# Kernel tuning notes

Hardware: AMD Instinct MI355X
Metric: run time of the kernel (lower is better)

The kernel has to match this reference:

```python
import jax, jax.numpy as jnp
from jax import lax
import numpy as np

# Dims matching init_kwargs / input_specs
B, R, C, CIN, COUT, W, CT = 8, 96, 64, 8, 64, 8, 4


def setup_inputs() -> dict:
    key = jax.random.key(0)
    ks = jax.random.split(key, 16)
    s = 0.05
    n = lambda k, shp: s * jax.random.normal(k, shp, jnp.float32)
    return {
        "x": jax.random.normal(ks[0], (B, R, C, CIN, 1), jnp.float32),
        "x_mark": jax.random.normal(ks[1], (B, R, C, CIN, CT), jnp.float32),
        # hidden_MLP_data: Conv1d(c_in -> c_in*c_out, k=W, groups=c_in) -> per-group in=1
        "Wd": n(ks[2], (CIN * COUT, 1, W)),
        "bd": n(ks[3], (CIN * COUT,)),
        # hidden_MLP_mark: Conv1d(c_in*CT -> c_in*c_out, k=W, groups=c_in) -> per-group in=CT
        "Wm": n(ks[4], (CIN * COUT, CT, W)),
        "bm": n(ks[5], (CIN * COUT,)),
        # gate_data: k=1 grouped conv, per-group 1 -> 2*c_out; stored einsum-friendly [g, 2*c_out]
        "Gd": n(ks[6], (CIN, 2 * COUT)),
        "bgd": n(ks[7], (CIN, 2 * COUT)),
        # gate_mark: per-group CT -> 2*c_out
        "Gm": n(ks[8], (CIN, 2 * COUT, CT)),
        "bgm": n(ks[9], (CIN, 2 * COUT)),
        # gate_hid: per-group c_out -> 2*c_out
        "Gh": n(ks[10], (CIN, 2 * COUT, COUT)),
        "bgh": n(ks[11], (CIN, 2 * COUT)),
        # fc: Conv1d(c_in*c_out -> c_in*c_out, k=seq_R, groups=c_in) -> [g, o, i, R]
        "Fw": n(ks[12], (CIN, COUT, COUT, R)),
        "bf": n(ks[13], (CIN, COUT)),
    }


def _grouped_conv1d(xa, w, b, groups):
    # xa: [N, Cin, L], w: [Cout, Cin//groups, K]
    y = lax.conv_general_dilated(
        xa, w, window_strides=(1,), padding="VALID",
        dimension_numbers=("NCH", "OIH", "NCH"), feature_group_count=groups)
    return y + b[None, :, None]


def reference(x, x_mark, Wd, bd, Wm, bm, Gd, bgd, Gm, bgm, Gh, bgh, Fw, bf):
    Bv, Rv, Cv, cin, _ = x.shape
    ct = x_mark.shape[-1]
    cout = Gh.shape[-1]
    Wk = Wd.shape[-1]

    # ---- deal(): causal windowed grouped conv over R ----
    # pad W zeros in front along R, drop last step -> length R+W-1, VALID conv k=W -> R
    xz = jnp.concatenate([jnp.zeros((Bv, Wk, Cv, cin, 1), x.dtype), x], axis=1)
    xa = xz.transpose(0, 2, 3, 4, 1).reshape(Bv * Cv, cin, Rv + Wk)[:, :, :-1]
    Hd = _grouped_conv1d(xa, Wd, bd, cin)  # [B*C, cin*cout, R]

    mz = jnp.concatenate([jnp.zeros((Bv, Wk, Cv, cin, ct), x.dtype), x_mark], axis=1)
    ma = mz.transpose(0, 2, 3, 4, 1).reshape(Bv * Cv, cin * ct, Rv + Wk)[:, :, :-1]
    Hm = _grouped_conv1d(ma, Wm, bm, cin)

    hid = (Hd + Hm).reshape(Bv, Cv, cin, cout, Rv).transpose(0, 4, 1, 2, 3)  # [B,R,C,cin,cout]

    # ---- gated_unit(): kernel-1 grouped convs == per-group matmuls ----
    xs = x[..., 0]  # [B,R,C,cin]
    g = jnp.einsum("brcg,go->brcgo", xs, Gd) + bgd
    g = g + jnp.einsum("brcgt,got->brcgo", x_mark, Gm) + bgm
    g = g + jnp.einsum("brcgi,goi->brcgo", hid, Gh) + bgh
    sg = jax.nn.sigmoid(g[..., :cout])
    tg = jnp.tanh(g[..., cout:])
    hid = hid * sg + (1.0 - sg) * tg  # [B,R,C,cin,cout]

    # ---- fc: grouped conv with kernel==R -> full contraction over (in-chan, R) ----
    out = jnp.einsum("brcgi,goir->bcgo", hid, Fw) + bf  # [B,C,cin,cout]
    return out
```

## Files before the change

kernel.cpp:

```cpp
#include <hip/hip_runtime.h>
#include <hip/hip_bf16.h>
#include <math.h>

namespace {

typedef __attribute__((ext_vector_type(8))) short bh8;
typedef __attribute__((ext_vector_type(4))) short sh4;
typedef __attribute__((ext_vector_type(4))) float fx4;

constexpr int Rn = 96, Cn = 64, CINn = 8, COUTn = 64;
constexpr int NPOS = 8 * 96 * 64 * 8;
constexpr int PPG  = 8 * 96 * 64;
constexpr float NLOG2E = -1.4426950408889634f;
constexpr float LOG2E2 =  2.8853900817779268f;
constexpr size_t FEAT_OFF = 0;
constexpr size_t FWT_OFF  = (size_t)NPOS * 16;
constexpr size_t CA_OFF   = FWT_OFF + (size_t)NPOS * 16;
constexpr size_t GWT_OFF  = CA_OFF + 65536;
constexpr size_t PART_OFF = GWT_OFF + 196608;

__device__ inline ushort f2b(float f) {
  __hip_bfloat16 h = __float2bfloat16(f);
  return __builtin_bit_cast(ushort, h);
}
__device__ inline int swz8(int bc, int rr, int ib) {
  return (bc * 1024 + rr * 128 + ib) ^ (((rr + bc) & 7) << 4);
}

#define MFMA16(a, b, c) __builtin_amdgcn_mfma_f32_16x16x32_bf16((a), (b), (c), 0, 0, 0)

__global__ __launch_bounds__(512)
void prep_k(const float* __restrict__ x, const float* __restrict__ xm,
            const float* __restrict__ Fw,
            const float* __restrict__ Gd, const float* __restrict__ bgd,
            const float* __restrict__ Gm, const float* __restrict__ bgm,
            const float* __restrict__ bgh,
            const float* __restrict__ Wd, const float* __restrict__ bd,
            const float* __restrict__ Wm, const float* __restrict__ bm,
            ushort* __restrict__ feat, ushort* __restrict__ FwT,
            ushort* __restrict__ GWT, ushort* __restrict__ cA)
{
  __shared__ float tile[64 * 97];
  const int bid = blockIdx.x, t = threadIdx.x;
  if (bid < 768) {
    const int pos = bid * 512 + t;
    const float xs = x[pos];
    const fx4 m = *(const fx4*)(xm + (size_t)pos * 4);
    bh8 o;
    o[0] = (short)f2b(xs);
    o[1] = (short)f2b(m[0]); o[2] = (short)f2b(m[1]);
    o[3] = (short)f2b(m[2]); o[4] = (short)f2b(m[3]);
    o[5] = (short)0x3F80; o[6] = 0; o[7] = 0;
    const int g = pos & 7, pb = pos >> 3;
    *(bh8*)(feat + ((size_t)g * PPG + pb) * 8) = o;
  } else if (bid < 1280) {
    const int go = bid - 768;
    const float* src = Fw + (size_t)go * 6144;
    ushort* dst = FwT + (size_t)go * 6144;
#pragma unroll
    for (int it = 0; it < 12; ++it) {
      const int idx = t + it * 512;
      tile[(idx / 96) * 97 + (idx % 96)] = src[idx];
    }
    __syncthreads();
#pragma unroll
    for (int it = 0; it < 12; ++it) {
      const int idx = t + it * 512;
      const int r = idx >> 6, i = idx & 63;
      dst[idx] = f2b(tile[i * 97 + r]);
    }
  } else if (bid < 1344) {
    const int e = (bid - 1280) * 512 + t;
    const int j = e & 7, lp = (e >> 3) & 63, sub = (e >> 9) & 7, g = e >> 12;
    const int il = lp >> 4, mr = lp & 15;
    const int o2 = (sub >> 2) * 64 + (sub & 3) * 16 + mr;
    float v = 0.f;
    if (il == 0) {
      if (j == 0)      v = Gd[g * 128 + o2];
      else if (j <= 4) v = Gm[(size_t)(g * 128 + o2) * 4 + (j - 1)];
      else if (j == 5) v = bgd[g * 128 + o2] + bgm[g * 128 + o2] + bgh[g * 128 + o2];
    }
    v *= (sub >= 4) ? LOG2E2 : NLOG2E;
    GWT[((size_t)(g * 24 + sub * 3 + 2) * 64 + lp) * 8 + j] = f2b(v);
  } else {
    const int e = (bid - 1344) * 512 + t;
    const int g = e >> 12, co = (e >> 6) & 63, k = e & 63;
    const int tap = k >> 3, tch = k & 7;
    float v = 0.f;
    if (tch == 0)      v = Wd[(g * 64 + co) * 8 + tap];
    else if (tch <= 4) v = Wm[((g * 64 + co) * 4 + (tch - 1)) * 8 + tap];
    else if (tch == 5 && tap == 0) v = bd[g * 64 + co] + bm[g * 64 + co];
    cA[e] = f2b(v);
  }
}

__global__ __launch_bounds__(256)
void gwk(const float* __restrict__ Gh, const float* __restrict__ Wd,
         const float* __restrict__ Wm, const float* __restrict__ bd,
         const float* __restrict__ bm, ushort* __restrict__ GWT)
{
  const int row = blockIdx.x * 4 + (threadIdx.x >> 6);
  const int k = threadIdx.x & 63;
  const int g = row >> 7, o2 = row & 127;
  const int tap = k >> 3, tch = k & 7;
  const float* pA; int sA = 0; float mA = 0.f, mB = 0.f;
  const float* pB;
  if (tch == 0)      { pA = Wd + (size_t)(g * 64) * 8 + tap; sA = 8;  mA = 1.f; }
  else if (tch <= 4) { pA = Wm + ((size_t)(g * 64) * 4 + (tch - 1)) * 8 + tap; sA = 32; mA = 1.f; }
  else if (tch == 5 && tap == 0) { pA = bd + g * 64; sA = 1; mA = 1.f; mB = 1.f; }
  else               { pA = Wd; }
  pB = (mB != 0.f) ? (bm + g * 64) : pA;
  const float* gh = Gh + (size_t)(g * 128 + o2) * 64;
  float acc = 0.f;
#pragma unroll 8
  for (int i = 0; i < 64; ++i) {
    const float wv = fmaf(mB, pB[i], mA * pA[i * sA]);
    acc = fmaf(gh[i], wv, acc);
  }
  acc *= (o2 >= 64) ? LOG2E2 : NLOG2E;
  const int half = o2 >> 6, s = (o2 >> 4) & 3, mr = o2 & 15;
  const int sub = half * 4 + s, fs = k >> 5, lp = ((k & 31) >> 3) * 16 + mr, j = k & 7;
  GWT[((size_t)(g * 24 + sub * 3 + fs) * 64 + lp) * 8 + j] = f2b(acc);
}

__global__ __launch_bounds__(512, 2)
void fused_v10(const ushort* __restrict__ feat, const ushort* __restrict__ FwT,
               const ushort* __restrict__ cA, const ushort* __restrict__ GWT,
               float* __restrict__ part)
{
  __shared__ __align__(16) ushort sTab[16384];
  __shared__ __align__(16) char sGat[2][16384];
  __shared__ float sRed[1024];

  const int t    = threadIdx.x;
  const int lane = t & 63;
  const int w    = t >> 6;
  const int il   = lane >> 4;
  const int mr   = lane & 15;
  const int bid  = blockIdx.x;
  const int g    = bid & 7;
  const int bcT  = (bid >> 3) & 31;
  const int chh  = bid >> 8;
  const ushort* fg = feat + (size_t)g * PPG * 8;
  const int s4   = w & 3, hf = w >> 2;
  const int tb   = lane * 8;

  const int pglob = w * 16 + mr;
  const int cbcl = pglob >> 3, crr = pglob & 7;
  const int cbcg = bcT * 16 + cbcl;
  const int cbb = cbcg >> 6, ccc = cbcg & 63;
  const size_t prow = (size_t)(cbb * 96) * 64 + ccc;

  *(bh8*)&sTab[w * 512 + tb] =
      *(const bh8*)(cA + g * 4096 + ((w >> 1) * 16 + mr) * 64 + (w & 1) * 32 + il * 8);
  {
    const ushort* gsrc = GWT + (size_t)g * 12288;
#pragma unroll
    for (int it = 0; it < 3; ++it) {
      const int idx = it * 512 + t;
      *(bh8*)&sTab[4096 + idx * 8] = *(const bh8*)(gsrc + idx * 8);
    }
  }

  int wadr[4];
#pragma unroll
  for (int s = 0; s < 4; ++s) wadr[s] = swz8(cbcl, crr, s * 32 + il * 8);
  const ushort* fb0 = FwT + ((size_t)(g * 64 + s4 * 16 + mr) * 96) * 64 + 32 * hf + 8 * il;

  fx4 facc = {0.f, 0.f, 0.f, 0.f};
  const bh8 zpad = {0, 0, 0, 0, 0, (short)0x3F80, 0, 0};

  bh8 b0, b1, bx;
  {
    const int r0 = chh * 48;
    const int q0 = r0 + crr - 8 + il;
    const int q1 = q0 + 4;
    b0 = *(const bh8*)(fg + (prow + (size_t)(q0 > 0 ? q0 : 0) * 64) * 8);
    b1 = *(const bh8*)(fg + (prow + (size_t)(q1 > 0 ? q1 : 0) * 64) * 8);
    bx = *(const bh8*)(fg + (prow + (size_t)(r0 + crr) * 64) * 8);
  }
  __syncthreads();

#pragma unroll 1
  for (int k6 = 0; k6 < 6; ++k6) {
    const int r0 = chh * 48 + k6 * 8;
    if (k6 == 0 && chh == 0) {
      if (crr - 8 + il < 0) b0 = zpad;
      if (crr - 4 + il < 0) b1 = zpad;
    }

    fx4 ah[4];
#pragma unroll
    for (int s = 0; s < 4; ++s) {
      const bh8 a0 = *(const bh8*)&sTab[(s * 2 + 0) * 512 + tb];
      const bh8 a1 = *(const bh8*)&sTab[(s * 2 + 1) * 512 + tb];
      fx4 a = {0.f, 0.f, 0.f, 0.f};
      a = MFMA16(a0, b0, a);
      a = MFMA16(a1, b1, a);
      ah[s] = a;
    }

    bh8 b0n = b0, b1n = b1, bxn = bx;
    if (k6 < 5) {
      const int qn = r0 + crr + il;
      b0n = *(const bh8*)(fg + (prow + (size_t)qn * 64) * 8);
      b1n = *(const bh8*)(fg + (prow + (size_t)(qn + 4) * 64) * 8);
      bxn = *(const bh8*)(fg + (prow + (size_t)(r0 + 8 + crr) * 64) * 8);
    }

    char* gbuf = sGat[k6 & 1];
#pragma unroll
    for (int s = 0; s < 4; ++s) {
      const int bs = (8 + s * 3) * 512 + tb;
      const int bt = (8 + (4 + s) * 3) * 512 + tb;
      fx4 aS = {0.f,0.f,0.f,0.f}, aT = {0.f,0.f,0.f,0.f};
      aS = MFMA16(*(const bh8*)&sTab[bs],        b0, aS);
      aS = MFMA16(*(const bh8*)&sTab[bs + 512],  b1, aS);
      aS = MFMA16(*(const bh8*)&sTab[bs + 1024], bx, aS);
      aT = MFMA16(*(const bh8*)&sTab[bt],        b0, aT);
      aT = MFMA16(*(const bh8*)&sTab[bt + 512],  b1, aT);
      aT = MFMA16(*(const bh8*)&sTab[bt + 1024], bx, aT);
      sh4 o4;
#pragma unroll
      for (int cc = 0; cc < 4; ++cc) {
        const float sig = __builtin_amdgcn_rcpf(1.f + exp2f(aS[cc]));
        const float y   = exp2f(aT[cc]);
        const float th  = (y - 1.f) * __builtin_amdgcn_rcpf(y + 1.f);
        o4[cc] = (short)f2b(fmaf(sig, ah[s][cc] - th, th));
      }
      *(sh4*)(gbuf + wadr[s]) = o4;
    }
    __syncthreads();

    {
      const ushort* fb = fb0 + (size_t)r0 * 64;
#pragma unroll
      for (int f = 0; f < 8; ++f) {
        const bh8 aF = *(const bh8*)(fb + f * 64);
        const bh8 bF = *(const bh8*)(gbuf + swz8(mr, f, 64 * hf + 16 * il));
        facc = MFMA16(aF, bF, facc);
      }
    }
    b0 = b0n; b1 = b1n; bx = bxn;
  }

  if (hf == 1) {
#pragma unroll
    for (int cc = 0; cc < 4; ++cc)
      sRed[s4 * 256 + (4 * il + cc) * 16 + mr] = facc[cc];
  }
  __syncthreads();
  if (hf == 0) {
    float* pp = part + ((size_t)(chh * 8 + g) * 32 + bcT) * 1024;
#pragma unroll
    for (int cc = 0; cc < 4; ++cc)
      pp[mr * 64 + s4 * 16 + 4 * il + cc] = facc[cc] + sRed[s4 * 256 + (4 * il + cc) * 16 + mr];
  }
}

__global__ __launch_bounds__(256)
void reduce_k(const float* __restrict__ part, const float* __restrict__ bf,
              float* __restrict__ out)
{
  const int e = blockIdx.x * 256 + threadIdx.x;
  const int o = e & 63, g = (e >> 6) & 7, bcg = e >> 9;
  const int bcT = bcg >> 4, bcl = bcg & 15;
  const float s = bf[g * 64 + o]
      + part[((size_t)(0 * 8 + g) * 32 + bcT) * 1024 + bcl * 64 + o]
      + part[((size_t)(1 * 8 + g) * 32 + bcT) * 1024 + bcl * 64 + o];
  out[e] = s;
}

}

extern "C" void kernel_launch(void* const* d_in, const int* in_sizes, int n_in,
                              void* d_out, int out_size, void* d_ws, size_t ws_size,
                              hipStream_t stream) {
  const float* x   = (const float*)d_in[0];
  const float* xm  = (const float*)d_in[1];
  const float* Wd  = (const float*)d_in[2];
  const float* bd  = (const float*)d_in[3];
  const float* Wm  = (const float*)d_in[4];
  const float* bm  = (const float*)d_in[5];
  const float* Gd  = (const float*)d_in[6];
  const float* bgd = (const float*)d_in[7];
  const float* Gm  = (const float*)d_in[8];
  const float* bgm = (const float*)d_in[9];
  const float* Gh  = (const float*)d_in[10];
  const float* bgh = (const float*)d_in[11];
  const float* Fw  = (const float*)d_in[12];
  const float* bf  = (const float*)d_in[13];
  float* outp = (float*)d_out;

  ushort* feat = (ushort*)((char*)d_ws + FEAT_OFF);
  ushort* FwT  = (ushort*)((char*)d_ws + FWT_OFF);
  ushort* cA   = (ushort*)((char*)d_ws + CA_OFF);
  ushort* GWT  = (ushort*)((char*)d_ws + GWT_OFF);
  float*  part = (float*)((char*)d_ws + PART_OFF);

  prep_k<<<dim3(1408), dim3(512), 0, stream>>>(
      x, xm, Fw, Gd, bgd, Gm, bgm, bgh, Wd, bd, Wm, bm, feat, FwT, GWT, cA);
  gwk<<<dim3(256), dim3(256), 0, stream>>>(Gh, Wd, Wm, bd, bm, GWT);
  fused_v10<<<dim3(512), dim3(512), 0, stream>>>(feat, FwT, cA, GWT, part);
  reduce_k<<<dim3(1024), dim3(256), 0, stream>>>(part, bf, outp);
}
```

Baseline: 57.61 us.

## Stage features through LDS double buffer, prefetch Fw early, merge gwk into prep

Merges the gwk weight-folding kernel into prep_k as extra blocks, which removes one kernel launch. In the fused kernel, each row's feature vectors are loaded once by 256 threads into a swizzled, double-buffered LDS tile. Previously every lane did three overlapping global loads per step. The FwT A-operands for the fc MFMA are now loaded at the top of each iteration so they overlap the gate computation. The trade-off is extra LDS and register pressure.

```diff
diff --git a/kernel.cpp b/kernel.cpp
--- a/kernel.cpp
+++ b/kernel.cpp
@@ -26,12 +26,15 @@
 __device__ inline int swz8(int bc, int rr, int ib) {
   return (bc * 1024 + rr * 128 + ib) ^ (((rr + bc) & 7) << 4);
 }
+__device__ inline int fswz(int l, int bc) {
+  return (l * 16 + (bc ^ (l & 7))) * 8;
+}
 
 #define MFMA16(a, b, c) __builtin_amdgcn_mfma_f32_16x16x32_bf16((a), (b), (c), 0, 0, 0)
 
 __global__ __launch_bounds__(512)
 void prep_k(const float* __restrict__ x, const float* __restrict__ xm,
-            const float* __restrict__ Fw,
+            const float* __restrict__ Fw, const float* __restrict__ Gh,
             const float* __restrict__ Gd, const float* __restrict__ bgd,
             const float* __restrict__ Gm, const float* __restrict__ bgm,
             const float* __restrict__ bgh,
@@ -82,7 +85,7 @@
     }
     v *= (sub >= 4) ? LOG2E2 : NLOG2E;
     GWT[((size_t)(g * 24 + sub * 3 + 2) * 64 + lp) * 8 + j] = f2b(v);
-  } else {
+  } else if (bid < 1408) {
     const int e = (bid - 1344) * 512 + t;
     const int g = e >> 12, co = (e >> 6) & 63, k = e & 63;
     const int tap = k >> 3, tch = k & 7;
@@ -91,45 +94,40 @@
     else if (tch <= 4) v = Wm[((g * 64 + co) * 4 + (tch - 1)) * 8 + tap];
     else if (tch == 5 && tap == 0) v = bd[g * 64 + co] + bm[g * 64 + co];
     cA[e] = f2b(v);
-  }
-}
-
-__global__ __launch_bounds__(256)
-void gwk(const float* __restrict__ Gh, const float* __restrict__ Wd,
-         const float* __restrict__ Wm, const float* __restrict__ bd,
-         const float* __restrict__ bm, ushort* __restrict__ GWT)
-{
-  const int row = blockIdx.x * 4 + (threadIdx.x >> 6);
-  const int k = threadIdx.x & 63;
-  const int g = row >> 7, o2 = row & 127;
-  const int tap = k >> 3, tch = k & 7;
-  const float* pA; int sA = 0; float mA = 0.f, mB = 0.f;
-  const float* pB;
-  if (tch == 0)      { pA = Wd + (size_t)(g * 64) * 8 + tap; sA = 8;  mA = 1.f; }
-  else if (tch <= 4) { pA = Wm + ((size_t)(g * 64) * 4 + (tch - 1)) * 8 + tap; sA = 32; mA = 1.f; }
-  else if (tch == 5 && tap == 0) { pA = bd + g * 64; sA = 1; mA = 1.f; mB = 1.f; }
-  else               { pA = Wd; }
-  pB = (mB != 0.f) ? (bm + g * 64) : pA;
-  const float* gh = Gh + (size_t)(g * 128 + o2) * 64;
-  float acc = 0.f;
+  } else {
+    const int e = (bid - 1408) * 512 + t;
+    const int row = e >> 6, k = e & 63;
+    const int g = row >> 7, o2 = row & 127;
+    const int tap = k >> 3, tch = k & 7;
+    const float* pA; int sA = 0; float mA = 0.f, mB = 0.f;
+    const float* pB;
+    if (tch == 0)      { pA = Wd + (size_t)(g * 64) * 8 + tap; sA = 8;  mA = 1.f; }
+    else if (tch <= 4) { pA = Wm + ((size_t)(g * 64) * 4 + (tch - 1)) * 8 + tap; sA = 32; mA = 1.f; }
+    else if (tch == 5 && tap == 0) { pA = bd + g * 64; sA = 1; mA = 1.f; mB = 1.f; }
+    else               { pA = Wd; }
+    pB = (mB != 0.f) ? (bm + g * 64) : pA;
+    const float* gh = Gh + (size_t)(g * 128 + o2) * 64;
+    float acc = 0.f;
 #pragma unroll 8
-  for (int i = 0; i < 64; ++i) {
-    const float wv = fmaf(mB, pB[i], mA * pA[i * sA]);
-    acc = fmaf(gh[i], wv, acc);
-  }
-  acc *= (o2 >= 64) ? LOG2E2 : NLOG2E;
-  const int half = o2 >> 6, s = (o2 >> 4) & 3, mr = o2 & 15;
-  const int sub = half * 4 + s, fs = k >> 5, lp = ((k & 31) >> 3) * 16 + mr, j = k & 7;
-  GWT[((size_t)(g * 24 + sub * 3 + fs) * 64 + lp) * 8 + j] = f2b(acc);
+    for (int i = 0; i < 64; ++i) {
+      const float wv = fmaf(mB, pB[i], mA * pA[i * sA]);
+      acc = fmaf(gh[i], wv, acc);
+    }
+    acc *= (o2 >= 64) ? LOG2E2 : NLOG2E;
+    const int half = o2 >> 6, s = (o2 >> 4) & 3, mr = o2 & 15;
+    const int sub = half * 4 + s, fs = k >> 5, lp = ((k & 31) >> 3) * 16 + mr, j = k & 7;
+    GWT[((size_t)(g * 24 + sub * 3 + fs) * 64 + lp) * 8 + j] = f2b(acc);
+  }
 }
 
 __global__ __launch_bounds__(512, 2)
-void fused_v10(const ushort* __restrict__ feat, const ushort* __restrict__ FwT,
+void fused_v11(const ushort* __restrict__ feat, const ushort* __restrict__ FwT,
                const ushort* __restrict__ cA, const ushort* __restrict__ GWT,
                float* __restrict__ part)
 {
   __shared__ __align__(16) ushort sTab[16384];
   __shared__ __align__(16) char sGat[2][16384];
+  __shared__ __align__(16) ushort sFeat[2][2048];
   __shared__ float sRed[1024];
 
   const int t    = threadIdx.x;
@@ -147,9 +145,12 @@
 
   const int pglob = w * 16 + mr;
   const int cbcl = pglob >> 3, crr = pglob & 7;
-  const int cbcg = bcT * 16 + cbcl;
-  const int cbb = cbcg >> 6, ccc = cbcg & 63;
-  const size_t prow = (size_t)(cbb * 96) * 64 + ccc;
+
+  const int sl = t >> 4, sbc = t & 15;
+  const int sbcg = bcT * 16 + sbc;
+  const size_t sprow = (size_t)((sbcg >> 6) * 96) * 64 + (sbcg & 63);
+  const int sadr = fswz(sl, sbc);
+  const bh8 zpad = {0, 0, 0, 0, 0, (short)0x3F80, 0, 0};
 
   *(bh8*)&sTab[w * 512 + tb] =
       *(const bh8*)(cA + g * 4096 + ((w >> 1) * 16 + mr) * 64 + (w & 1) * 32 + il * 8);
@@ -161,33 +162,42 @@
       *(bh8*)&sTab[4096 + idx * 8] = *(const bh8*)(gsrc + idx * 8);
     }
   }
-
+  if (t < 256) {
+    const int q = chh * 48 - 8 + sl;
+    *(bh8*)&sFeat[0][sadr] =
+        (q >= 0) ? *(const bh8*)(fg + (sprow + (size_t)q * 64) * 8) : zpad;
+  }
+
+  const int a_b0 = fswz(crr + il, cbcl);
+  const int a_b1 = fswz(crr + il + 4, cbcl);
+  const int a_bx = fswz(crr + 8, cbcl);
   int wadr[4];
 #pragma unroll
   for (int s = 0; s < 4; ++s) wadr[s] = swz8(cbcl, crr, s * 32 + il * 8);
   const ushort* fb0 = FwT + ((size_t)(g * 64 + s4 * 16 + mr) * 96) * 64 + 32 * hf + 8 * il;
 
   fx4 facc = {0.f, 0.f, 0.f, 0.f};
-  const bh8 zpad = {0, 0, 0, 0, 0, (short)0x3F80, 0, 0};
-
-  bh8 b0, b1, bx;
-  {
-    const int r0 = chh * 48;
-    const int q0 = r0 + crr - 8 + il;
-    const int q1 = q0 + 4;
-    b0 = *(const bh8*)(fg + (prow + (size_t)(q0 > 0 ? q0 : 0) * 64) * 8);
-    b1 = *(const bh8*)(fg + (prow + (size_t)(q1 > 0 ? q1 : 0) * 64) * 8);
-    bx = *(const bh8*)(fg + (prow + (size_t)(r0 + crr) * 64) * 8);
-  }
   __syncthreads();
 
+  int cur = 0;
 #pragma unroll 1
   for (int k6 = 0; k6 < 6; ++k6) {
     const int r0 = chh * 48 + k6 * 8;
-    if (k6 == 0 && chh == 0) {
-      if (crr - 8 + il < 0) b0 = zpad;
-      if (crr - 4 + il < 0) b1 = zpad;
-    }
+
+    bh8 stg;
+    const bool do_stage = (t < 256) && (k6 < 5);
+    if (do_stage)
+      stg = *(const bh8*)(fg + (sprow + (size_t)(r0 + sl) * 64) * 8);
+    bh8 aF[8];
+    {
+      const ushort* fb = fb0 + (size_t)r0 * 64;
+#pragma unroll
+      for (int f = 0; f < 8; ++f) aF[f] = *(const bh8*)(fb + f * 64);
+    }
+
+    const bh8 b0 = *(const bh8*)&sFeat[cur][a_b0];
+    const bh8 b1 = *(const bh8*)&sFeat[cur][a_b1];
+    const bh8 bx = *(const bh8*)&sFeat[cur][a_bx];
 
     fx4 ah[4];
 #pragma unroll
@@ -198,14 +208,6 @@
       a = MFMA16(a0, b0, a);
       a = MFMA16(a1, b1, a);
       ah[s] = a;
-    }
-
-    bh8 b0n = b0, b1n = b1, bxn = bx;
-    if (k6 < 5) {
-      const int qn = r0 + crr + il;
-      b0n = *(const bh8*)(fg + (prow + (size_t)qn * 64) * 8);
-      b1n = *(const bh8*)(fg + (prow + (size_t)(qn + 4) * 64) * 8);
-      bxn = *(const bh8*)(fg + (prow + (size_t)(r0 + 8 + crr) * 64) * 8);
     }
 
     char* gbuf = sGat[k6 & 1];
@@ -230,18 +232,16 @@
       }
       *(sh4*)(gbuf + wadr[s]) = o4;
     }
+
+    if (do_stage) *(bh8*)&sFeat[cur ^ 1][sadr] = stg;
     __syncthreads();
 
-    {
-      const ushort* fb = fb0 + (size_t)r0 * 64;
-#pragma unroll
-      for (int f = 0; f < 8; ++f) {
-        const bh8 aF = *(const bh8*)(fb + f * 64);
-        const bh8 bF = *(const bh8*)(gbuf + swz8(mr, f, 64 * hf + 16 * il));
-        facc = MFMA16(aF, bF, facc);
-      }
-    }
-    b0 = b0n; b1 = b1n; bx = bxn;
+#pragma unroll
+    for (int f = 0; f < 8; ++f) {
+      const bh8 bF = *(const bh8*)(gbuf + swz8(mr, f, 64 * hf + 16 * il));
+      facc = MFMA16(aF[f], bF, facc);
+    }
+    cur ^= 1;
   }
 
   if (hf == 1) {
@@ -298,9 +298,8 @@
   ushort* GWT  = (ushort*)((char*)d_ws + GWT_OFF);
   float*  part = (float*)((char*)d_ws + PART_OFF);
 
-  prep_k<<<dim3(1408), dim3(512), 0, stream>>>(
-      x, xm, Fw, Gd, bgd, Gm, bgm, bgh, Wd, bd, Wm, bm, feat, FwT, GWT, cA);
-  gwk<<<dim3(256), dim3(256), 0, stream>>>(Gh, Wd, Wm, bd, bm, GWT);
-  fused_v10<<<dim3(512), dim3(512), 0, stream>>>(feat, FwT, cA, GWT, part);
+  prep_k<<<dim3(1536), dim3(512), 0, stream>>>(
+      x, xm, Fw, Gh, Gd, bgd, Gm, bgm, bgh, Wd, bd, Wm, bm, feat, FwT, GWT, cA);
+  fused_v11<<<dim3(512), dim3(512), 0, stream>>>(feat, FwT, cA, GWT, part);
   reduce_k<<<dim3(1024), dim3(256), 0, stream>>>(part, bf, outp);
 }
```

After: 56.03 us. 2.7% less time.
